# Optimization experiments

Hardware: AMD Instinct MI355X
Metric: run time of the kernel (lower is better)

Reference implementation:

```python
import jax, jax.numpy as jnp
import numpy as np

B, S, D, H = 2, 2048, 1024, 16
DEPTH = D // H


def setup_inputs() -> dict:
    key = jax.random.key(0)
    ks = jax.random.split(key, 10)
    batch = jax.random.normal(ks[0], (B, S, D), dtype=jnp.float32)
    # variable-length valid rows, like padded batches in the original repo
    lengths = jax.random.randint(ks[1], (B,), S // 2, S + 1)
    mask = jnp.arange(S)[None, :] < lengths[:, None]  # (B, S) bool
    scale = 1.0 / np.sqrt(D)
    Wq = jax.random.normal(ks[2], (D, D), dtype=jnp.float32) * scale
    bq = jnp.zeros((D,), dtype=jnp.float32)
    Wk = jax.random.normal(ks[3], (D, D), dtype=jnp.float32) * scale
    bk = jnp.zeros((D,), dtype=jnp.float32)
    Wv = jax.random.normal(ks[4], (D, D), dtype=jnp.float32) * scale
    bv = jnp.zeros((D,), dtype=jnp.float32)
    Wo = jax.random.normal(ks[5], (D, D), dtype=jnp.float32) * scale
    bo = jnp.zeros((D,), dtype=jnp.float32)
    return {"batch": batch, "mask": mask, "Wq": Wq, "bq": bq, "Wk": Wk,
            "bk": bk, "Wv": Wv, "bv": bv, "Wo": Wo, "bo": bo}


def _split_heads(x):
    # (B, S, D) -> (B, H, S, depth)
    b, s, _ = x.shape
    return x.reshape(b, s, H, DEPTH).transpose(0, 2, 1, 3)


def reference(batch, mask, Wq, bq, Wk, bk, Wv, bv, Wo, bo):
    b, s, _ = batch.shape
    Q = _split_heads(batch @ Wq + bq)
    K = _split_heads(batch @ Wk + bk)
    V = _split_heads(batch @ Wv + bv)
    # scaled dot-product attention with key-padding mask
    logits = jnp.einsum('bhqd,bhkd->bhqk', Q, K) / jnp.sqrt(
        jnp.asarray(DEPTH, dtype=batch.dtype))
    neg = (~mask).astype(batch.dtype) * -1e9  # (B, S)
    logits = logits + neg[:, None, None, :]
    attn = jax.nn.softmax(logits, axis=-1)
    X = jnp.einsum('bhqk,bhkd->bhqd', attn, V)
    X = X.transpose(0, 2, 1, 3).reshape(b, s, D)
    return X @ Wo + bo
```

## Files before the change

kernel.cpp:

```cpp
#include <hip/hip_runtime.h>
#include <hip/hip_bf16.h>

#define DEV __device__ __forceinline__

typedef short bf16x8 __attribute__((ext_vector_type(8)));
typedef float f32x4  __attribute__((ext_vector_type(4)));
typedef float f32x16 __attribute__((ext_vector_type(16)));

#define Bc 2
#define Sc 2048
#define Dc 1024
#define Hc 16

#define OFF_XB    0u
#define OFF_WQKVT 8388608u
#define OFF_WOT   14680064u
#define OFF_Q     16777216u
#define OFF_K     25165824u
#define OFF_VT    33554432u
#define OFF_XA    41943040u
#define OFF_BIASC 50331648u
#define OFF_LENS  50343936u

DEV short f2bf(float f) {
    __hip_bfloat16 h = __float2bfloat16(f);
    union { __hip_bfloat16 h; short s; } u; u.h = h; return u.s;
}

DEV int cvtpk(float lo, float hi_) {
    int r;
    asm("v_cvt_pk_bf16_f32 %0, %1, %2" : "=v"(r) : "v"(lo), "v"(hi_));
    return r;
}

DEV void gload16(const void* g, void* l) {
    __builtin_amdgcn_global_load_lds((const __attribute__((address_space(1))) void*)g,
                                     (__attribute__((address_space(3))) void*)l, 16, 0, 0);
}

union I4BF { int i[4]; bf16x8 v; };

DEV bf16x8 vread(const char* Vc, int row, int kkbyte, int hi8, int rsw) {
    union { short4 h[2]; bf16x8 v; } u;
    u.h[0] = *(const short4*)(Vc + row * 128 + ((kkbyte + hi8) ^ rsw));
    u.h[1] = *(const short4*)(Vc + row * 128 + ((kkbyte + 16 + hi8) ^ rsw));
    return u.v;
}


__global__ void cast_bf16_kernel(const float* __restrict__ in, short* __restrict__ out, int n4) {
    int i = blockIdx.x * blockDim.x + threadIdx.x;
    if (i >= n4) return;
    float4 v = ((const float4*)in)[i];
    short4 o;
    o.x = f2bf(v.x); o.y = f2bf(v.y); o.z = f2bf(v.z); o.w = f2bf(v.w);
    ((short4*)out)[i] = o;
}

__global__ void wtrans_kernel(const float* __restrict__ Wq, const float* __restrict__ Wk,
                              const float* __restrict__ Wv, const float* __restrict__ Wo,
                              short* __restrict__ WQKVT, short* __restrict__ WOT) {
    const float* src; short* dst;
    int z = blockIdx.z;
    if (z == 0)      { src = Wq; dst = WQKVT; }
    else if (z == 1) { src = Wk; dst = WQKVT + 1024 * 1024; }
    else if (z == 2) { src = Wv; dst = WQKVT + 2 * 1024 * 1024; }
    else             { src = Wo; dst = WOT; }
    __shared__ float t[32][33];
    int tx = threadIdx.x, ty = threadIdx.y;
    int r0 = blockIdx.y * 32, c0 = blockIdx.x * 32;
#pragma unroll
    for (int i = 0; i < 4; i++)
        t[ty + i * 8][tx] = src[(size_t)(r0 + ty + i * 8) * Dc + c0 + tx];
    __syncthreads();
#pragma unroll
    for (int i = 0; i < 4; i++)
        dst[(size_t)(c0 + ty + i * 8) * Dc + r0 + tx] = f2bf(t[tx][ty + i * 8]);
}

__global__ void prep_small_kernel(const float* __restrict__ bq, const float* __restrict__ bk,
                                  const float* __restrict__ bv,
                                  const unsigned char* __restrict__ mask,
                                  float* __restrict__ biasc, int* __restrict__ lens) {
    int blk = blockIdx.x, t = threadIdx.x;
    if (blk == 0) {
        if (t < Dc) { biasc[t] = bq[t]; biasc[Dc + t] = bk[t]; biasc[2 * Dc + t] = bv[t]; }
        return;
    }
    int b = blk - 1;
    bool is_i32 = (mask[1] == 0);
    __shared__ int cnt;
    if (t == 0) cnt = 0;
    __syncthreads();
    int local = 0;
    for (int s = t; s < Sc; s += blockDim.x) {
        bool v = is_i32 ? (((const int*)mask)[b * Sc + s] != 0) : (mask[b * Sc + s] != 0);
        local += v ? 1 : 0;
    }
    atomicAdd(&cnt, local);
    __syncthreads();
    if (t == 0) lens[b] = cnt;
}

__global__ __launch_bounds__(256) void vtrans_kernel(const short* __restrict__ V,
                                                     short* __restrict__ VT) {
    __shared__ short t[64][65];
    int tid = threadIdx.x;
    int bh = blockIdx.y, s0 = blockIdx.x * 64;
    int rr = tid >> 2, c4 = (tid & 3) * 16;
    const short* vrow = V + ((size_t)bh * Sc + s0 + rr) * 64 + c4;
    *(bf16x8*)&t[rr][c4]     = *(const bf16x8*)(vrow);
    *(bf16x8*)&t[rr][c4 + 8] = *(const bf16x8*)(vrow + 8);
    __syncthreads();
    bf16x8 a, b2;
#pragma unroll
    for (int i = 0; i < 8; i++) { a[i] = t[c4 + i][rr]; b2[i] = t[c4 + 8 + i][rr]; }
    short* orow = VT + ((size_t)bh * 64 + rr) * Sc + s0 + c4;
    *(bf16x8*)(orow)     = a;
    *(bf16x8*)(orow + 8) = b2;
}

__global__ __launch_bounds__(256) void gemm_qkv_kernel(
    const short* __restrict__ A, const short* __restrict__ BT, const float* __restrict__ bias,
    short* __restrict__ Qp, short* __restrict__ Kp, short* __restrict__ Vp)
{
    __shared__ short As[128 * 32];
    __shared__ short Bs[128 * 32];
    int tid = threadIdx.x, lane = tid & 63, wave = tid >> 6;
    int l15 = lane & 15, lhi = lane >> 4;
    int bm = blockIdx.x, bn = blockIdx.y;
    int wm = wave >> 1, wn = wave & 1;

    const f32x4 fzero = {0.f, 0.f, 0.f, 0.f};
    f32x4 acc[4][4];
#pragma unroll
    for (int i = 0; i < 4; i++)
#pragma unroll
        for (int j = 0; j < 4; j++) acc[i][j] = fzero;

    const char* Ab = (const char*)A;
    const char* Bb = (const char*)BT;

    for (int k0 = 0; k0 < 1024; k0 += 32) {
#pragma unroll
        for (int i = 0; i < 2; i++) {
            int o = wave * 2048 + i * 1024 + lane * 16;
            int row = o >> 6, cb = o & 63;
            gload16(Ab + ((size_t)(bm * 128 + row) * 1024 + k0) * 2 + cb,
                    (char*)As + wave * 2048 + i * 1024);
            gload16(Bb + ((size_t)(bn * 128 + row) * 1024 + k0) * 2 + cb,
                    (char*)Bs + wave * 2048 + i * 1024);
        }
        __syncthreads();
        bf16x8 af[4], bfv[4];
#pragma unroll
        for (int i = 0; i < 4; i++) {
            af[i]  = *(const bf16x8*)(As + (wm * 64 + i * 16 + l15) * 32 + lhi * 8);
            bfv[i] = *(const bf16x8*)(Bs + (wn * 64 + i * 16 + l15) * 32 + lhi * 8);
        }
#pragma unroll
        for (int i = 0; i < 4; i++)
#pragma unroll
            for (int j = 0; j < 4; j++)
                acc[i][j] = __builtin_amdgcn_mfma_f32_16x16x32_bf16(af[i], bfv[j], acc[i][j], 0, 0, 0);
        __syncthreads();
    }

#pragma unroll
    for (int i = 0; i < 4; i++)
#pragma unroll
        for (int j = 0; j < 4; j++) {
            int c = bn * 128 + wn * 64 + j * 16 + l15;
            float bc = bias[c];
            int rb = bm * 128 + wm * 64 + i * 16 + 4 * lhi;
#pragma unroll
            for (int reg = 0; reg < 4; reg++) {
                int r = rb + reg;
                float v = acc[i][j][reg] + bc;
                int which = c >> 10, cc = c & 1023, h = cc >> 6, d = cc & 63;
                int b = r >> 11, s = r & 2047;
                int bh = b * Hc + h;
                if (which == 0) v *= 0.18033688f;
                short sv = f2bf(v);
                size_t idx = ((size_t)bh * Sc + s) * 64 + d;
                if (which == 0)      Qp[idx] = sv;
                else if (which == 1) Kp[idx] = sv;
                else                 Vp[idx] = sv;
            }
        }
}

__global__ __launch_bounds__(256) void gemm_out_kernel(
    const short* __restrict__ A, const short* __restrict__ BT, const float* __restrict__ bias,
    float* __restrict__ outF)
{
    __shared__ short As[128 * 32];
    __shared__ short Bs[64 * 32];
    int tid = threadIdx.x, lane = tid & 63, wave = tid >> 6;
    int l15 = lane & 15, lhi = lane >> 4;
    int bm = blockIdx.x, bn = blockIdx.y;

    const f32x4 fzero = {0.f, 0.f, 0.f, 0.f};
    f32x4 acc[2][4];
#pragma unroll
    for (int i = 0; i < 2; i++)
#pragma unroll
        for (int j = 0; j < 4; j++) acc[i][j] = fzero;

    const char* Ab = (const char*)A;
    const char* Bb = (const char*)BT;

    for (int k0 = 0; k0 < 1024; k0 += 32) {
#pragma unroll
        for (int i = 0; i < 2; i++) {
            int o = wave * 2048 + i * 1024 + lane * 16;
            int row = o >> 6, cb = o & 63;
            gload16(Ab + ((size_t)(bm * 128 + row) * 1024 + k0) * 2 + cb,
                    (char*)As + wave * 2048 + i * 1024);
        }
        {
            int o = wave * 1024 + lane * 16;
            int row = o >> 6, cb = o & 63;
            gload16(Bb + ((size_t)(bn * 64 + row) * 1024 + k0) * 2 + cb,
                    (char*)Bs + wave * 1024);
        }
        __syncthreads();
        bf16x8 af[2], bfv[4];
#pragma unroll
        for (int i = 0; i < 2; i++)
            af[i] = *(const bf16x8*)(As + (wave * 32 + i * 16 + l15) * 32 + lhi * 8);
#pragma unroll
        for (int j = 0; j < 4; j++)
            bfv[j] = *(const bf16x8*)(Bs + (j * 16 + l15) * 32 + lhi * 8);
#pragma unroll
        for (int i = 0; i < 2; i++)
#pragma unroll
            for (int j = 0; j < 4; j++)
                acc[i][j] = __builtin_amdgcn_mfma_f32_16x16x32_bf16(af[i], bfv[j], acc[i][j], 0, 0, 0);
        __syncthreads();
    }

#pragma unroll
    for (int i = 0; i < 2; i++)
#pragma unroll
        for (int j = 0; j < 4; j++) {
            int c = bn * 64 + j * 16 + l15;
            float bc = bias[c];
            int rb = bm * 128 + wave * 32 + i * 16 + 4 * lhi;
#pragma unroll
            for (int reg = 0; reg < 4; reg++)
                outF[(size_t)(rb + reg) * Dc + c] = acc[i][j][reg] + bc;
        }
}

__global__ __launch_bounds__(256) void attn_kernel(
    const short* __restrict__ Qp, const short* __restrict__ Kp, const short* __restrict__ VTp,
    const int* __restrict__ lens, short* __restrict__ Xout)
{
    __shared__ short Kt[2][64 * 64];
    __shared__ short Vt[2][64 * 64];
    int tid = threadIdx.x, lane = tid & 63, wave = tid >> 6;
    int l31 = lane & 31, hi = lane >> 5;
    int bh = blockIdx.y, b = bh >> 4, h = bh & 15;
    int q0 = blockIdx.x * 128 + wave * 32;

    const short* Qb  = Qp + (size_t)bh * Sc * 64;
    const char*  Kb  = (const char*)(Kp + (size_t)bh * Sc * 64);
    const char*  VTb = (const char*)(VTp + (size_t)bh * 64 * Sc);

    bf16x8 qf[4];
#pragma unroll
    for (int kk = 0; kk < 4; kk++)
        qf[kk] = *(const bf16x8*)(Qb + (size_t)(q0 + l31) * 64 + kk * 16 + hi * 8);

    f32x16 xacc0, xacc1;
#pragma unroll
    for (int r = 0; r < 16; r++) { xacc0[r] = 0.f; xacc1[r] = 0.f; }
    float lreg = 0.f;

    int len = lens[b];
    int nt = (len + 63) >> 6;
    int rsw = (l31 & 7) << 4;
    int hi8 = hi * 8;

#define STAGE(bufi, kt_)                                                              \
    {                                                                                 \
        int k0_ = (kt_) * 64;                                                         \
        _Pragma("unroll")                                                             \
        for (int i = 0; i < 2; i++) {                                                 \
            int o = wave * 2048 + i * 1024 + lane * 16;                               \
            int row = o >> 7, cb = o & 127;                                           \
            int scb = cb ^ ((row & 7) << 4);                                          \
            gload16(Kb + (size_t)(k0_ + row) * 128 + scb,                             \
                    (char*)&Kt[bufi][0] + wave * 2048 + i * 1024);                    \
            gload16(VTb + (size_t)row * (Sc * 2) + (size_t)k0_ * 2 + scb,             \
                    (char*)&Vt[bufi][0] + wave * 2048 + i * 1024);                    \
        }                                                                             \
    }

#define DOHALF(Kc, Vc, ROFF, KBASE, KT)                                               \
    {                                                                                 \
        f32x16 s;                                                                     \
        _Pragma("unroll")                                                             \
        for (int r = 0; r < 16; r++) s[r] = 0.f;                                      \
        __builtin_amdgcn_s_setprio(1);                                                \
        _Pragma("unroll")                                                             \
        for (int kk = 0; kk < 4; kk++) {                                              \
            bf16x8 kf = *(const bf16x8*)((Kc) + (ROFF + l31) * 128 +                  \
                                         ((kk * 32 + hi * 16) ^ rsw));                \
            s = __builtin_amdgcn_mfma_f32_32x32x16_bf16(kf, qf[kk], s, 0, 0, 0);      \
        }                                                                             \
        __builtin_amdgcn_s_setprio(0);                                                \
        if ((KT) == nt - 1) {                                                         \
            int rem = len - (KT) * 64;                                                \
            if (rem < (KBASE) + 32) {                                                 \
                _Pragma("unroll")                                                     \
                for (int r = 0; r < 16; r++) {                                        \
                    int key0 = (KBASE) + 4 * hi + (r & 3) + 8 * (r >> 2);             \
                    if (key0 >= rem) s[r] = -3.0e38f;                                 \
                }                                                                     \
            }                                                                         \
        }                                                                             \
        _Pragma("unroll")                                                             \
        for (int r = 0; r < 16; r++) { s[r] = exp2f(s[r]); lreg += s[r]; }            \
        I4BF u, w;                                                                    \
        u.i[0] = cvtpk(s[0], s[1]);   u.i[1] = cvtpk(s[2], s[3]);                     \
        u.i[2] = cvtpk(s[4], s[5]);   u.i[3] = cvtpk(s[6], s[7]);                     \
        w.i[0] = cvtpk(s[8], s[9]);   w.i[1] = cvtpk(s[10], s[11]);                   \
        w.i[2] = cvtpk(s[12], s[13]); w.i[3] = cvtpk(s[14], s[15]);                   \
        __builtin_amdgcn_s_setprio(1);                                                \
        {                                                                             \
            bf16x8 v0 = vread((Vc), l31,      (KBASE) * 2,      hi8, rsw);            \
            bf16x8 v1 = vread((Vc), 32 + l31, (KBASE) * 2,      hi8, rsw);            \
            xacc0 = __builtin_amdgcn_mfma_f32_32x32x16_bf16(v0, u.v, xacc0, 0, 0, 0); \
            xacc1 = __builtin_amdgcn_mfma_f32_32x32x16_bf16(v1, u.v, xacc1, 0, 0, 0); \
            bf16x8 v2 = vread((Vc), l31,      (KBASE) * 2 + 32, hi8, rsw);            \
            bf16x8 v3 = vread((Vc), 32 + l31, (KBASE) * 2 + 32, hi8, rsw);            \
            xacc0 = __builtin_amdgcn_mfma_f32_32x32x16_bf16(v2, w.v, xacc0, 0, 0, 0); \
            xacc1 = __builtin_amdgcn_mfma_f32_32x32x16_bf16(v3, w.v, xacc1, 0, 0, 0); \
        }                                                                             \
        __builtin_amdgcn_s_setprio(0);                                                \
    }

#define DOTILE(BUFI, KT)                                                              \
    {                                                                                 \
        const char* Kc_ = (const char*)&Kt[BUFI][0];                                  \
        const char* Vc_ = (const char*)&Vt[BUFI][0];                                  \
        DOHALF(Kc_, Vc_, 0, 0, KT);                                                   \
        DOHALF(Kc_, Vc_, 32, 32, KT);                                                 \
    }

    STAGE(0, 0);
    __syncthreads();

    int kt = 0;
    while (kt + 2 <= nt) {
        if (kt + 1 < nt) STAGE(1, kt + 1);
        DOTILE(0, kt);
        __syncthreads();
        if (kt + 2 < nt) STAGE(0, kt + 2);
        DOTILE(1, kt + 1);
        __syncthreads();
        kt += 2;
    }
    if (kt < nt) DOTILE(0, kt);

    float lfull = lreg + __shfl_xor(lreg, 32, 64);
    float rl = 1.0f / lfull;
    short* orow = Xout + (size_t)(b * Sc + q0 + l31) * Dc + h * 64;
#pragma unroll
    for (int g = 0; g < 4; g++) {
        short4 o;
        o.x = f2bf(xacc0[4 * g + 0] * rl);
        o.y = f2bf(xacc0[4 * g + 1] * rl);
        o.z = f2bf(xacc0[4 * g + 2] * rl);
        o.w = f2bf(xacc0[4 * g + 3] * rl);
        *(short4*)(orow + 4 * hi + 8 * g) = o;
    }
#pragma unroll
    for (int g = 0; g < 4; g++) {
        short4 o;
        o.x = f2bf(xacc1[4 * g + 0] * rl);
        o.y = f2bf(xacc1[4 * g + 1] * rl);
        o.z = f2bf(xacc1[4 * g + 2] * rl);
        o.w = f2bf(xacc1[4 * g + 3] * rl);
        *(short4*)(orow + 32 + 4 * hi + 8 * g) = o;
    }
}


extern "C" void kernel_launch(void* const* d_in, const int* in_sizes, int n_in,
                              void* d_out, int out_size, void* d_ws, size_t ws_size,
                              hipStream_t stream) {
    const float* batch = (const float*)d_in[0];
    const unsigned char* mask = (const unsigned char*)d_in[1];
    const float* Wq = (const float*)d_in[2];
    const float* bq = (const float*)d_in[3];
    const float* Wk = (const float*)d_in[4];
    const float* bk = (const float*)d_in[5];
    const float* Wv = (const float*)d_in[6];
    const float* bv = (const float*)d_in[7];
    const float* Wo = (const float*)d_in[8];
    const float* bo = (const float*)d_in[9];

    char* ws = (char*)d_ws;
    short* XB    = (short*)(ws + OFF_XB);
    short* WQKVT = (short*)(ws + OFF_WQKVT);
    short* WOT   = (short*)(ws + OFF_WOT);
    short* Qb    = (short*)(ws + OFF_Q);
    short* Kb    = (short*)(ws + OFF_K);
    short* VTb   = (short*)(ws + OFF_VT);
    short* XAb   = (short*)(ws + OFF_XA);
    float* BIASC = (float*)(ws + OFF_BIASC);
    int*   LENS  = (int*)(ws + OFF_LENS);
    short* Vscr  = (short*)d_out;

    cast_bf16_kernel<<<4096, 256, 0, stream>>>(batch, XB, 1048576);
    wtrans_kernel<<<dim3(32, 32, 4), dim3(32, 8), 0, stream>>>(Wq, Wk, Wv, Wo, WQKVT, WOT);
    prep_small_kernel<<<3, 1024, 0, stream>>>(bq, bk, bv, mask, BIASC, LENS);

    gemm_qkv_kernel<<<dim3(32, 24), 256, 0, stream>>>(XB, WQKVT, BIASC, Qb, Kb, Vscr);
    vtrans_kernel<<<dim3(32, 32), 256, 0, stream>>>(Vscr, VTb);
    attn_kernel<<<dim3(16, 32), 256, 0, stream>>>(Qb, Kb, VTb, LENS, XAb);
    gemm_out_kernel<<<dim3(32, 16), 256, 0, stream>>>(XAb, WOT, bo, (float*)d_out);
}
```

Measured before the change: 137.9 us.

## Split attention key range across two blocks and merge partials in a combine kernel

Attention now launches twice as many blocks, each covering half of the valid key tiles. Each block writes unnormalized fp32 partial outputs and row sums to workspace, and a new combine kernel adds them, normalizes and writes the bf16 result. A block-index swizzle is also added to change the scheduling order. The goal is more parallelism than the original 512 blocks give on a large GPU. The cost is extra fp32 traffic and one more kernel launch. Merging the halves by plain addition is only correct if both halves share a softmax reference (for example a fixed max), which the hidden code must provide.

```diff
diff --git a/kernel.cpp b/kernel.cpp
--- a/kernel.cpp
+++ b/kernel.cpp
@@ -14,13 +14,16 @@
 
 #define OFF_XB    0u
 #define OFF_WQKVT 8388608u
-#define OFF_WOT   14680064u
-#define OFF_Q     16777216u
-#define OFF_K     25165824u
-#define OFF_VT    33554432u
-#define OFF_XA    41943040u
-#define OFF_BIASC 50331648u
-#define OFF_LENS  50343936u
+#define OFF_PX1   0u
+#define OFF_WOT   16777216u
+#define OFF_Q     18874368u
+#define OFF_K     27262976u
+#define OFF_VT    35651584u
+#define OFF_XA    44040192u
+#define OFF_BIASC 52428800u
+#define OFF_LENS  52441088u
+#define OFF_PL0   52441152u
+#define OFF_PL1   52703296u
 
 DEV short f2bf(float f) {
     __hip_bfloat16 h = __float2bfloat16(f);
@@ -255,14 +258,21 @@
 
 __global__ __launch_bounds__(256) void attn_kernel(
     const short* __restrict__ Qp, const short* __restrict__ Kp, const short* __restrict__ VTp,
-    const int* __restrict__ lens, short* __restrict__ Xout)
+    const int* __restrict__ lens,
+    float* __restrict__ PX0, float* __restrict__ PX1,
+    float* __restrict__ PL0, float* __restrict__ PL1)
 {
+    int tid = threadIdx.x, lane = tid & 63, wave = tid >> 6;
+    int l31 = lane & 31, hi = lane >> 5;
+
+    int orig = blockIdx.x;
+    int swz = (orig & 7) * 128 + (orig >> 3);
+    int bx = swz & 15, bh = (swz >> 4) & 31, sp = swz >> 9;
+    int b = bh >> 4;
+    int q0 = bx * 128 + wave * 32;
+
     __shared__ short Kt[2][64 * 64];
     __shared__ short Vt[2][64 * 64];
-    int tid = threadIdx.x, lane = tid & 63, wave = tid >> 6;
-    int l31 = lane & 31, hi = lane >> 5;
-    int bh = blockIdx.y, b = bh >> 4, h = bh & 15;
-    int q0 = blockIdx.x * 128 + wave * 32;
 
     const short* Qb  = Qp + (size_t)bh * Sc * 64;
     const char*  Kb  = (const char*)(Kp + (size_t)bh * Sc * 64);
@@ -280,6 +290,8 @@
 
     int len = lens[b];
     int nt = (len + 63) >> 6;
+    int half = (nt + 1) >> 1;
+    int t0 = sp ? half : 0, t1 = sp ? nt : half;
     int rsw = (l31 & 7) << 4;
     int hi8 = hi * 8;
 
@@ -350,42 +362,57 @@
         DOHALF(Kc_, Vc_, 32, 32, KT);                                                 \
     }
 
-    STAGE(0, 0);
+    STAGE(0, t0);
     __syncthreads();
 
-    int kt = 0;
-    while (kt + 2 <= nt) {
-        if (kt + 1 < nt) STAGE(1, kt + 1);
+    int kt = t0;
+    while (kt + 2 <= t1) {
+        if (kt + 1 < t1) STAGE(1, kt + 1);
         DOTILE(0, kt);
         __syncthreads();
-        if (kt + 2 < nt) STAGE(0, kt + 2);
+        if (kt + 2 < t1) STAGE(0, kt + 2);
         DOTILE(1, kt + 1);
         __syncthreads();
         kt += 2;
     }
-    if (kt < nt) DOTILE(0, kt);
+    if (kt < t1) DOTILE(0, kt);
 
     float lfull = lreg + __shfl_xor(lreg, 32, 64);
-    float rl = 1.0f / lfull;
-    short* orow = Xout + (size_t)(b * Sc + q0 + l31) * Dc + h * 64;
+    size_t qidx = (size_t)bh * Sc + q0 + l31;
+    float* prow = (sp ? PX1 : PX0) + qidx * 64;
 #pragma unroll
     for (int g = 0; g < 4; g++) {
-        short4 o;
-        o.x = f2bf(xacc0[4 * g + 0] * rl);
-        o.y = f2bf(xacc0[4 * g + 1] * rl);
-        o.z = f2bf(xacc0[4 * g + 2] * rl);
-        o.w = f2bf(xacc0[4 * g + 3] * rl);
-        *(short4*)(orow + 4 * hi + 8 * g) = o;
+        float4 o = make_float4(xacc0[4 * g + 0], xacc0[4 * g + 1],
+                               xacc0[4 * g + 2], xacc0[4 * g + 3]);
+        *(float4*)(prow + 4 * hi + 8 * g) = o;
     }
 #pragma unroll
     for (int g = 0; g < 4; g++) {
-        short4 o;
-        o.x = f2bf(xacc1[4 * g + 0] * rl);
-        o.y = f2bf(xacc1[4 * g + 1] * rl);
-        o.z = f2bf(xacc1[4 * g + 2] * rl);
-        o.w = f2bf(xacc1[4 * g + 3] * rl);
-        *(short4*)(orow + 32 + 4 * hi + 8 * g) = o;
-    }
+        float4 o = make_float4(xacc1[4 * g + 0], xacc1[4 * g + 1],
+                               xacc1[4 * g + 2], xacc1[4 * g + 3]);
+        *(float4*)(prow + 32 + 4 * hi + 8 * g) = o;
+    }
+    if (hi == 0) (sp ? PL1 : PL0)[qidx] = lfull;
+}
+
+__global__ __launch_bounds__(256) void combine_kernel(
+    const float* __restrict__ PX0, const float* __restrict__ PX1,
+    const float* __restrict__ PL0, const float* __restrict__ PL1,
+    short* __restrict__ XA)
+{
+    int i = blockIdx.x * 256 + threadIdx.x;
+    int qidx = i >> 4, quad = i & 15;
+    const float4 a = ((const float4*)PX0)[i];
+    const float4 c = ((const float4*)PX1)[i];
+    float rl = 1.0f / (PL0[qidx] + PL1[qidx]);
+    int bh = qidx >> 11, qrow = qidx & 2047;
+    int b = bh >> 4, h = bh & 15;
+    short4 o;
+    o.x = f2bf((a.x + c.x) * rl);
+    o.y = f2bf((a.y + c.y) * rl);
+    o.z = f2bf((a.z + c.z) * rl);
+    o.w = f2bf((a.w + c.w) * rl);
+    *(short4*)(XA + (size_t)(b * Sc + qrow) * Dc + h * 64 + quad * 4) = o;
 }
 
 
@@ -406,6 +433,7 @@
     char* ws = (char*)d_ws;
     short* XB    = (short*)(ws + OFF_XB);
     short* WQKVT = (short*)(ws + OFF_WQKVT);
+    float* PX1   = (float*)(ws + OFF_PX1);
     short* WOT   = (short*)(ws + OFF_WOT);
     short* Qb    = (short*)(ws + OFF_Q);
     short* Kb    = (short*)(ws + OFF_K);
@@ -413,7 +441,10 @@
     short* XAb   = (short*)(ws + OFF_XA);
     float* BIASC = (float*)(ws + OFF_BIASC);
     int*   LENS  = (int*)(ws + OFF_LENS);
+    float* PL0   = (float*)(ws + OFF_PL0);
+    float* PL1   = (float*)(ws + OFF_PL1);
     short* Vscr  = (short*)d_out;
+    float* PX0   = (float*)d_out;
 
     cast_bf16_kernel<<<4096, 256, 0, stream>>>(batch, XB, 1048576);
     wtrans_kernel<<<dim3(32, 32, 4), dim3(32, 8), 0, stream>>>(Wq, Wk, Wv, Wo, WQKVT, WOT);
@@ -421,6 +452,7 @@
 
     gemm_qkv_kernel<<<dim3(32, 24), 256, 0, stream>>>(XB, WQKVT, BIASC, Qb, Kb, Vscr);
     vtrans_kernel<<<dim3(32, 32), 256, 0, stream>>>(Vscr, VTb);
-    attn_kernel<<<dim3(16, 32), 256, 0, stream>>>(Qb, Kb, VTb, LENS, XAb);
+    attn_kernel<<<1024, 256, 0, stream>>>(Qb, Kb, VTb, LENS, PX0, PX1, PL0, PL1);
+    combine_kernel<<<4096, 256, 0, stream>>>(PX0, PX1, PL0, PL1, XAb);
     gemm_out_kernel<<<dim3(32, 16), 256, 0, stream>>>(XAb, WOT, bo, (float*)d_out);
 }
```

After: 149.4 us. 1.08x slower.
